# Performance work log

Measured on AMD Instinct MI355X. Metric: run time of the kernel, lower is better.

## Reference

```python
import jax, jax.numpy as jnp
import numpy as np

N_NODES = 100000
N_EDGES = 1600000
N_GRAPHS = 1000
H = 4

def _ln(x, g, b, eps=1e-5):
    m = x.mean(-1, keepdims=True)
    v = ((x - m) ** 2).mean(-1, keepdims=True)
    return (x - m) / jnp.sqrt(v + eps) * g + b

def _gat(x, src, dst, W, att_src, att_dst, bias, C):
    # PyG GATConv (self-loops already appended to src/dst): per-edge scores,
    # segment softmax over incoming edges of each dst node, scatter-add aggregation.
    N = x.shape[0]
    h = (x @ W.T).reshape(N, H, C)                      # [N,H,C]
    a_s = (h * att_src[None]).sum(-1)                   # [N,H]
    a_d = (h * att_dst[None]).sum(-1)                   # [N,H]
    e = jax.nn.leaky_relu(a_s[src] + a_d[dst], 0.2)     # [E,H]
    m = jax.ops.segment_max(e, dst, num_segments=N)
    w = jnp.exp(e - m[dst])
    denom = jax.ops.segment_sum(w, dst, num_segments=N)
    alpha = w / denom[dst]
    out = jax.ops.segment_sum(alpha[:, :, None] * h[src], dst, num_segments=N)
    return out.reshape(N, H * C) + bias

def _mha_len1(y, in_w, in_b, out_w, out_b, d):
    # seq_len==1 (x.unsqueeze(0)): softmax over a single key is identically 1,
    # so MHA(y,y,y) == out_proj(v_proj(y)). Exactly the original math.
    v = y @ in_w[2 * d:3 * d].T + in_b[2 * d:3 * d]
    return v @ out_w.T + out_b

def _forward(x, edge_index, batch, fc_feat_w, fc_feat_b,
             gat1_w, gat1_as, gat1_ad, gat1_b,
             gat2_w, gat2_as, gat2_ad, gat2_b,
             enc_in_w, enc_in_b, enc_out_w, enc_out_b,
             enc_f1_w, enc_f1_b, enc_f2_w, enc_f2_b,
             enc_ln1_g, enc_ln1_b, enc_ln2_g, enc_ln2_b,
             dec_sa_in_w, dec_sa_in_b, dec_sa_out_w, dec_sa_out_b,
             dec_ca_in_w, dec_ca_in_b, dec_ca_out_w, dec_ca_out_b,
             dec_f1_w, dec_f1_b, dec_f2_w, dec_f2_b,
             dec_ln1_g, dec_ln1_b, dec_ln2_g, dec_ln2_b, dec_ln3_g, dec_ln3_b,
             fc_w, fc_b):
    N = x.shape[0]
    d = 16 * H  # 64
    loop = jnp.arange(N, dtype=edge_index.dtype)
    src = jnp.concatenate([edge_index[0], loop])  # add_self_loops=True (PyG default)
    dst = jnp.concatenate([edge_index[1], loop])
    h = x @ fc_feat_w.T + fc_feat_b                     # feature_fc: [N,8]
    h = jax.nn.leaky_relu(_gat(h, src, dst, gat1_w, gat1_as, gat1_ad, gat1_b, 32), 0.01)
    h = jax.nn.leaky_relu(_gat(h, src, dst, gat2_w, gat2_as, gat2_ad, gat2_b, 16), 0.01)
    y = h  # [N,64]; transformer sees (L=1, B=N, E=64)
    for i in range(2):  # encoder layers
        a = _mha_len1(y, enc_in_w[i], enc_in_b[i], enc_out_w[i], enc_out_b[i], d)
        y = _ln(y + a, enc_ln1_g[i], enc_ln1_b[i])
        f = jax.nn.relu(y @ enc_f1_w[i].T + enc_f1_b[i]) @ enc_f2_w[i].T + enc_f2_b[i]
        y = _ln(y + f, enc_ln2_g[i], enc_ln2_b[i])
    for i in range(2):  # decoder layers (memory == tgt)
        a = _mha_len1(y, dec_sa_in_w[i], dec_sa_in_b[i], dec_sa_out_w[i], dec_sa_out_b[i], d)
        y = _ln(y + a, dec_ln1_g[i], dec_ln1_b[i])
        a = _mha_len1(y, dec_ca_in_w[i], dec_ca_in_b[i], dec_ca_out_w[i], dec_ca_out_b[i], d)
        y = _ln(y + a, dec_ln2_g[i], dec_ln2_b[i])
        f = jax.nn.relu(y @ dec_f1_w[i].T + dec_f1_b[i]) @ dec_f2_w[i].T + dec_f2_b[i]
        y = _ln(y + f, dec_ln3_g[i], dec_ln3_b[i])
    sums = jax.ops.segment_sum(y, batch, num_segments=N_GRAPHS)
    cnts = jax.ops.segment_sum(jnp.ones((N,), y.dtype), batch, num_segments=N_GRAPHS)
    pooled = sums / jnp.maximum(cnts, 1.0)[:, None]     # global_mean_pool
    return pooled @ fc_w.T + fc_b

def setup_inputs() -> dict:
    key = jax.random.key(0)
    ks = iter(jax.random.split(key, 64))
    p = lambda *s: jax.random.normal(next(ks), s, dtype=jnp.float32) * 0.1
    d = 64
    inp = {
        'x': jax.random.normal(next(ks), (N_NODES, 4), dtype=jnp.float32),
        'edge_index': jax.random.randint(next(ks), (2, N_EDGES), 0, N_NODES, dtype=jnp.int32),
        'batch': jnp.sort(jax.random.randint(next(ks), (N_NODES,), 0, N_GRAPHS, dtype=jnp.int32)),
        'fc_feat_w': p(8, 4), 'fc_feat_b': p(8),
        'gat1_w': p(128, 8), 'gat1_as': p(H, 32), 'gat1_ad': p(H, 32), 'gat1_b': p(128),
        'gat2_w': p(64, 128), 'gat2_as': p(H, 16), 'gat2_ad': p(H, 16), 'gat2_b': p(64),
        'enc_in_w': p(2, 3 * d, d), 'enc_in_b': p(2, 3 * d), 'enc_out_w': p(2, d, d), 'enc_out_b': p(2, d),
        'enc_f1_w': p(2, 256, d), 'enc_f1_b': p(2, 256), 'enc_f2_w': p(2, d, 256), 'enc_f2_b': p(2, d),
        'enc_ln1_g': jnp.ones((2, d)), 'enc_ln1_b': jnp.zeros((2, d)),
        'enc_ln2_g': jnp.ones((2, d)), 'enc_ln2_b': jnp.zeros((2, d)),
        'dec_sa_in_w': p(2, 3 * d, d), 'dec_sa_in_b': p(2, 3 * d), 'dec_sa_out_w': p(2, d, d), 'dec_sa_out_b': p(2, d),
        'dec_ca_in_w': p(2, 3 * d, d), 'dec_ca_in_b': p(2, 3 * d), 'dec_ca_out_w': p(2, d, d), 'dec_ca_out_b': p(2, d),
        'dec_f1_w': p(2, 256, d), 'dec_f1_b': p(2, 256), 'dec_f2_w': p(2, d, 256), 'dec_f2_b': p(2, d),
        'dec_ln1_g': jnp.ones((2, d)), 'dec_ln1_b': jnp.zeros((2, d)),
        'dec_ln2_g': jnp.ones((2, d)), 'dec_ln2_b': jnp.zeros((2, d)),
        'dec_ln3_g': jnp.ones((2, d)), 'dec_ln3_b': jnp.zeros((2, d)),
        'fc_w': p(33, d), 'fc_b': p(33),
    }
    return inp

def reference(x, edge_index, batch, fc_feat_w, fc_feat_b,
              gat1_w, gat1_as, gat1_ad, gat1_b,
              gat2_w, gat2_as, gat2_ad, gat2_b,
              enc_in_w, enc_in_b, enc_out_w, enc_out_b,
              enc_f1_w, enc_f1_b, enc_f2_w, enc_f2_b,
              enc_ln1_g, enc_ln1_b, enc_ln2_g, enc_ln2_b,
              dec_sa_in_w, dec_sa_in_b, dec_sa_out_w, dec_sa_out_b,
              dec_ca_in_w, dec_ca_in_b, dec_ca_out_w, dec_ca_out_b,
              dec_f1_w, dec_f1_b, dec_f2_w, dec_f2_b,
              dec_ln1_g, dec_ln1_b, dec_ln2_g, dec_ln2_b, dec_ln3_g, dec_ln3_b,
              fc_w, fc_b):
    return _forward(x, edge_index, batch, fc_feat_w, fc_feat_b,
                    gat1_w, gat1_as, gat1_ad, gat1_b,
                    gat2_w, gat2_as, gat2_ad, gat2_b,
                    enc_in_w, enc_in_b, enc_out_w, enc_out_b,
                    enc_f1_w, enc_f1_b, enc_f2_w, enc_f2_b,
                    enc_ln1_g, enc_ln1_b, enc_ln2_g, enc_ln2_b,
                    dec_sa_in_w, dec_sa_in_b, dec_sa_out_w, dec_sa_out_b,
                    dec_ca_in_w, dec_ca_in_b, dec_ca_out_w, dec_ca_out_b,
                    dec_f1_w, dec_f1_b, dec_f2_w, dec_f2_b,
                    dec_ln1_g, dec_ln1_b, dec_ln2_g, dec_ln2_b, dec_ln3_g, dec_ln3_b,
                    fc_w, fc_b)
```

## Files before the change

### kernel.cpp

```cpp
#include <hip/hip_runtime.h>

#define NN 100000
#define NE 1600000
#define NG 1000
#define ETOT (NE + NN)
#define NODES_PER_GRP 12500

typedef _Float16 f16x8 __attribute__((ext_vector_type(8)));
typedef _Float16 f16x4 __attribute__((ext_vector_type(4)));
typedef _Float16 f16x2 __attribute__((ext_vector_type(2)));
typedef float f32x16 __attribute__((ext_vector_type(16)));
#define XROW 72

__global__ void k_h1(const float* __restrict__ x, const float* __restrict__ ffw,
                     const float* __restrict__ ffb, const float* __restrict__ g1w,
                     const float* __restrict__ asw, const float* __restrict__ adw,
                     _Float16* __restrict__ h1p, float* __restrict__ asp,
                     float* __restrict__ ad_, int* __restrict__ deg) {
    int tid = blockIdx.x * 256 + threadIdx.x;
    if (tid < NN) deg[tid] = 0;
    int n = __builtin_amdgcn_readfirstlane(tid >> 6);
    int jp = threadIdx.x & 63;
    float xv[4];
#pragma unroll
    for (int k = 0; k < 4; k++) xv[k] = x[n * 4 + k];
    float h0[8];
#pragma unroll
    for (int o = 0; o < 8; o++) {
        float a = ffb[o];
#pragma unroll
        for (int k = 0; k < 4; k++) a = fmaf(xv[k], ffw[o * 4 + k], a);
        h0[o] = a;
    }
    const float* w0 = g1w + jp * 8;
    const float* w1 = g1w + (jp + 64) * 8;
    float a0 = 0.f, a1 = 0.f;
#pragma unroll
    for (int k = 0; k < 8; k++) { a0 = fmaf(h0[k], w0[k], a0); a1 = fmaf(h0[k], w1[k], a1); }
    f16x2 r; r[0] = (_Float16)a0; r[1] = (_Float16)a1;
    *(f16x2*)(h1p + ((size_t)n * 64 + jp) * 2) = r;
    float p0 = a0 * asw[jp], p1 = a1 * asw[jp + 64];
    float d0 = a0 * adw[jp], d1 = a1 * adw[jp + 64];
#pragma unroll
    for (int m = 1; m <= 16; m <<= 1) {
        p0 += __shfl_xor(p0, m, 64); p1 += __shfl_xor(p1, m, 64);
        d0 += __shfl_xor(d0, m, 64); d1 += __shfl_xor(d1, m, 64);
    }
    if ((jp & 31) == 0) {
        int half = jp >> 5;
        *(float2*)(asp + n * 4 + half * 2) = make_float2(p0, p1);
        ad_[n * 4 + half] = d0;
        ad_[n * 4 + 2 + half] = d1;
    }
}

#define CLD(q) int ee##q = e + q * stride; \
               int d##q = (ee##q < NE) ? __builtin_nontemporal_load(ei + NE + ee##q) : -1;
#define CAT(q) if (d##q >= lo && d##q < hi) atomicAdd(&deg[d##q], 1);
__global__ void k_count(const int* __restrict__ ei, int* __restrict__ deg) {
    int g = blockIdx.x & 7;
    int bi = blockIdx.x >> 3;
    int nb = gridDim.x >> 3;
    int lo = g * NODES_PER_GRP, hi = lo + NODES_PER_GRP;
    int stride = nb * 256;
    for (int e = bi * 256 + threadIdx.x; e < NE; e += 8 * stride) {
        CLD(0) CLD(1) CLD(2) CLD(3) CLD(4) CLD(5) CLD(6) CLD(7)
        CAT(0) CAT(1) CAT(2) CAT(3) CAT(4) CAT(5) CAT(6) CAT(7)
    }
}

__global__ void k_scan1(const int* __restrict__ deg, int* __restrict__ offs, int* __restrict__ bsum) {
    __shared__ int s[1024];
    int tid = threadIdx.x;
    int i = blockIdx.x * 1024 + tid;
    int v = (i < NN) ? deg[i] + 1 : 0;
    s[tid] = v;
    __syncthreads();
    for (int d = 1; d < 1024; d <<= 1) {
        int t = 0;
        if (tid >= d) t = s[tid - d];
        __syncthreads();
        if (tid >= d) s[tid] += t;
        __syncthreads();
    }
    if (i < NN) offs[i] = s[tid] - v;
    if (tid == 1023) bsum[blockIdx.x] = s[tid];
}

__global__ void k_scan2(int* __restrict__ bsum) {
    __shared__ int s[128];
    int tid = threadIdx.x;
    int v = (tid < 98) ? bsum[tid] : 0;
    s[tid] = v;
    __syncthreads();
    for (int d = 1; d < 128; d <<= 1) {
        int t = 0;
        if (tid >= d) t = s[tid - d];
        __syncthreads();
        if (tid >= d) s[tid] += t;
        __syncthreads();
    }
    bsum[tid] = s[tid] - v;
}

__global__ void k_scan3(int* __restrict__ offs, const int* __restrict__ bsum, int* __restrict__ cur,
                        int* __restrict__ srcs) {
    int i = blockIdx.x * 1024 + threadIdx.x;
    if (i < NN) {
        int v = offs[i] + bsum[blockIdx.x];
        offs[i] = v;
        cur[i] = v + 1;
        srcs[v] = i;
    }
    if (i == 0) offs[NN] = ETOT;
}

#define SLD(q) int ee##q = e + q * stride; int d##q = -1, s##q = 0; \
               if (ee##q < NE) { d##q = __builtin_nontemporal_load(ei + NE + ee##q); \
                                 s##q = __builtin_nontemporal_load(ei + ee##q); }
#define SAT(q) if (d##q >= lo && d##q < hi) { int p = atomicAdd(&cur[d##q], 1); srcs[p] = s##q; }
__global__ void k_scatter(const int* __restrict__ ei, int* __restrict__ cur,
                          int* __restrict__ srcs) {
    int g = blockIdx.x & 7;
    int bi = blockIdx.x >> 3;
    int nb = gridDim.x >> 3;
    int lo = g * NODES_PER_GRP, hi = lo + NODES_PER_GRP;
    int stride = nb * 256;
    for (int e = bi * 256 + threadIdx.x; e < NE; e += 8 * stride) {
        SLD(0) SLD(1) SLD(2) SLD(3) SLD(4) SLD(5) SLD(6) SLD(7)
        SAT(0) SAT(1) SAT(2) SAT(3) SAT(4) SAT(5) SAT(6) SAT(7)
    }
}

__global__ void k_ew1(const int* __restrict__ offs, const int* __restrict__ srcs,
                      const float* __restrict__ asp, const float* __restrict__ ad_,
                      uint2* __restrict__ ew) {
    int t = blockIdx.x * 256 + threadIdx.x;
    int d = t >> 4, li = t & 15;
    if (d >= NN) return;
    int off = offs[d], deg = offs[d + 1] - off;
    float4 b = *(const float4*)(ad_ + d * 4);
    for (int j = li; j < deg; j += 16) {
        int s = srcs[off + j];
        float4 a = *(const float4*)(asp + s * 4);
        float e0 = a.x + b.x; e0 = fmaxf(e0, 0.2f * e0);
        float e2 = a.y + b.z; e2 = fmaxf(e2, 0.2f * e2);
        float e1 = a.z + b.y; e1 = fmaxf(e1, 0.2f * e1);
        float e3 = a.w + b.w; e3 = fmaxf(e3, 0.2f * e3);
        union { unsigned u; _Float16 h[2]; } c0, c1;
        c0.h[0] = (_Float16)__expf(e0); c0.h[1] = (_Float16)__expf(e2);
        c1.h[0] = (_Float16)__expf(e1); c1.h[1] = (_Float16)__expf(e3);
        uint2 o; o.x = c0.u; o.y = c1.u;
        ew[off + j] = o;
    }
}

__global__ void k_ew2(const int* __restrict__ offs, const int* __restrict__ srcs,
                      const float* __restrict__ as_, const float* __restrict__ ad_,
                      uint2* __restrict__ ew) {
    int t = blockIdx.x * 256 + threadIdx.x;
    int d = t >> 4, li = t & 15;
    if (d >= NN) return;
    int off = offs[d], deg = offs[d + 1] - off;
    float4 b = *(const float4*)(ad_ + d * 4);
    for (int j = li; j < deg; j += 16) {
        int s = srcs[off + j];
        float4 a = *(const float4*)(as_ + s * 4);
        float e0 = a.x + b.x; e0 = fmaxf(e0, 0.2f * e0);
        float e1 = a.y + b.y; e1 = fmaxf(e1, 0.2f * e1);
        float e2 = a.z + b.z; e2 = fmaxf(e2, 0.2f * e2);
        float e3 = a.w + b.w; e3 = fmaxf(e3, 0.2f * e3);
        union { unsigned u; _Float16 h[2]; } c0, c1;
        c0.h[0] = (_Float16)__expf(e0); c0.h[1] = (_Float16)__expf(e1);
        c1.h[0] = (_Float16)__expf(e2); c1.h[1] = (_Float16)__expf(e3);
        uint2 o; o.x = c0.u; o.y = c1.u;
        ew[off + j] = o;
    }
}

#define G1LD(q)  int s##q = sp[j + q]; uint2 e##q = wp[j + q];
#define G1LDM(q) int jj##q = j + q; int jc##q = jj##q < deg ? jj##q : deg - 1; \
                 int s##q = sp[jc##q]; uint2 e##q = wp[jc##q]; \
                 if (jj##q >= deg) { e##q.x = 0u; e##q.y = 0u; }
#define G1GA(q)  f16x2 p##q = *(const f16x2*)(h1p + (size_t)s##q * 128 + lane * 2);
#define G1AC(q, W0, W1, A0, A1) { \
    union { unsigned u; _Float16 h[2]; } c; c.u = hA ? e##q.y : e##q.x; \
    float w0 = (float)c.h[0], w1 = (float)c.h[1]; \
    W0 += w0; W1 += w1; \
    A0 = fmaf(w0, (float)p##q[0], A0); A1 = fmaf(w1, (float)p##q[1], A1); }

__global__ void k_gat1(const int* __restrict__ offs, const int* __restrict__ srcs,
                       const uint2* __restrict__ ew, const _Float16* __restrict__ h1p,
                       const float* __restrict__ bias, _Float16* __restrict__ g1h) {
    int wid = __builtin_amdgcn_readfirstlane((blockIdx.x * 256 + threadIdx.x) >> 6);
    int lane = threadIdx.x & 63;
    if (wid >= NN) return;
    int off = offs[wid];
    int deg = offs[wid + 1] - off;
    int hA = lane >> 5;
    const int* sp = srcs + off;
    const uint2* wp = ew + off;
    float ws0 = 0.f, ws1 = 0.f, ac0 = 0.f, ac1 = 0.f;
    float ws0b = 0.f, ws1b = 0.f, ac0b = 0.f, ac1b = 0.f;
    int j = 0;
    for (; j + 8 <= deg; j += 8) {
        G1LD(0) G1LD(1) G1LD(2) G1LD(3) G1LD(4) G1LD(5) G1LD(6) G1LD(7)
        G1GA(0) G1GA(1) G1GA(2) G1GA(3) G1GA(4) G1GA(5) G1GA(6) G1GA(7)
        G1AC(0, ws0, ws1, ac0, ac1)     G1AC(1, ws0b, ws1b, ac0b, ac1b)
        G1AC(2, ws0, ws1, ac0, ac1)     G1AC(3, ws0b, ws1b, ac0b, ac1b)
        G1AC(4, ws0, ws1, ac0, ac1)     G1AC(5, ws0b, ws1b, ac0b, ac1b)
        G1AC(6, ws0, ws1, ac0, ac1)     G1AC(7, ws0b, ws1b, ac0b, ac1b)
    }
    if (j < deg) {
        G1LDM(0) G1LDM(1) G1LDM(2) G1LDM(3) G1LDM(4) G1LDM(5) G1LDM(6) G1LDM(7)
        G1GA(0) G1GA(1) G1GA(2) G1GA(3) G1GA(4) G1GA(5) G1GA(6) G1GA(7)
        G1AC(0, ws0, ws1, ac0, ac1)     G1AC(1, ws0b, ws1b, ac0b, ac1b)
        G1AC(2, ws0, ws1, ac0, ac1)     G1AC(3, ws0b, ws1b, ac0b, ac1b)
        G1AC(4, ws0, ws1, ac0, ac1)     G1AC(5, ws0b, ws1b, ac0b, ac1b)
        G1AC(6, ws0, ws1, ac0, ac1)     G1AC(7, ws0b, ws1b, ac0b, ac1b)
    }
    ws0 += ws0b; ws1 += ws1b; ac0 += ac0b; ac1 += ac1b;
    float v0 = ac0 / ws0 + bias[lane];      v0 = fmaxf(v0, 0.01f * v0);
    float v1 = ac1 / ws1 + bias[lane + 64]; v1 = fmaxf(v1, 0.01f * v1);
    g1h[(size_t)wid * 128 + lane] = (_Float16)v0;
    g1h[(size_t)wid * 128 + lane + 64] = (_Float16)v1;
}

#define G2LD(q)  int s##q = sp[j + q]; uint2 e##q = wp[j + q];
#define G2LDM(q) int jj##q = j + q; int jc##q = jj##q < deg ? jj##q : deg - 1; \
                 int s##q = sp[jc##q]; uint2 e##q = wp[jc##q]; \
                 if (jj##q >= deg) { e##q.x = 0u; e##q.y = 0u; }
#define G2GA(q)  float hv##q = (float)h2h[(size_t)s##q * 64 + lane];
#define G2AC(q, W, A) { \
    unsigned sel = (hd & 2) ? e##q.y : e##q.x; \
    union { unsigned u; _Float16 h[2]; } c; c.u = sel >> sh; \
    float w = (float)c.h[0]; W += w; A = fmaf(w, hv##q, A); }

__global__ void k_gat2(const int* __restrict__ offs, const int* __restrict__ srcs,
                       const uint2* __restrict__ ew, const _Float16* __restrict__ h2h,
                       const float* __restrict__ bias, _Float16* __restrict__ g2h) {
    int wid = __builtin_amdgcn_readfirstlane((blockIdx.x * 256 + threadIdx.x) >> 6);
    int lane = threadIdx.x & 63;
    if (wid >= NN) return;
    int off = offs[wid];
    int deg = offs[wid + 1] - off;
    int hd = lane >> 4;
    int sh = (hd & 1) * 16;
    const int* sp = srcs + off;
    const uint2* wp = ew + off;
    float ws = 0.f, ac = 0.f, wsb = 0.f, acb = 0.f;
    int j = 0;
    for (; j + 8 <= deg; j += 8) {
        G2LD(0) G2LD(1) G2LD(2) G2LD(3) G2LD(4) G2LD(5) G2LD(6) G2LD(7)
        G2GA(0) G2GA(1) G2GA(2) G2GA(3) G2GA(4) G2GA(5) G2GA(6) G2GA(7)
        G2AC(0, ws, ac)  G2AC(1, wsb, acb)
        G2AC(2, ws, ac)  G2AC(3, wsb, acb)
        G2AC(4, ws, ac)  G2AC(5, wsb, acb)
        G2AC(6, ws, ac)  G2AC(7, wsb, acb)
    }
    if (j < deg) {
        G2LDM(0) G2LDM(1) G2LDM(2) G2LDM(3) G2LDM(4) G2LDM(5) G2LDM(6) G2LDM(7)
        G2GA(0) G2GA(1) G2GA(2) G2GA(3) G2GA(4) G2GA(5) G2GA(6) G2GA(7)
        G2AC(0, ws, ac)  G2AC(1, wsb, acb)
        G2AC(2, ws, ac)  G2AC(3, wsb, acb)
        G2AC(4, ws, ac)  G2AC(5, wsb, acb)
        G2AC(6, ws, ac)  G2AC(7, wsb, acb)
    }
    ws += wsb; ac += acb;
    float v = ac / ws + bias[lane]; v = fmaxf(v, 0.01f * v);
    g2h[(size_t)wid * 64 + lane] = (_Float16)v;
}

#define GROW 136
#define CROW 72
__global__ __launch_bounds__(256, 2) void k_h2m(const _Float16* __restrict__ g1h,
                                                const _Float16* __restrict__ apw2,
                                                const float* __restrict__ asw,
                                                const float* __restrict__ adw,
                                                _Float16* __restrict__ h2h,
                                                float* __restrict__ as_,
                                                float* __restrict__ ad_) {
    __shared__ _Float16 ls[4 * 32 * GROW];
    const int t = threadIdx.x;
    const int w = t >> 6, l = t & 63;
    const int col = l & 31, hf = l >> 5;
    const int wv = blockIdx.x * 4 + w;
    const int nb = wv * 32;
    if (nb >= NN) return;
    _Float16* g16 = ls + w * (32 * GROW);
    const int r = l >> 1, hb = l & 1;
    {
        int nr = nb + r; if (nr >= NN) nr = NN - 1;
        const _Float16* src = g1h + (size_t)nr * 128 + hb * 64;
        _Float16* dst = g16 + r * GROW + hb * 64;
#pragma unroll
        for (int q = 0; q < 8; q++)
            *(f16x8*)(dst + q * 8) = *(const f16x8*)(src + q * 8);
    }
    f16x8 bf[8];
#pragma unroll
    for (int ks = 0; ks < 8; ks++)
        bf[ks] = *(const f16x8*)(g16 + col * GROW + ks * 16 + hf * 8);
    f32x16 acc0, acc1;
#pragma unroll
    for (int i = 0; i < 16; i++) { acc0[i] = 0.f; acc1[i] = 0.f; }
#pragma unroll
    for (int ks = 0; ks < 8; ks++) {
        f16x8 a0 = *(const f16x8*)(apw2 + ((0 * 8 + ks) * 64 + l) * 8);
        f16x8 a1 = *(const f16x8*)(apw2 + ((1 * 8 + ks) * 64 + l) * 8);
        acc0 = __builtin_amdgcn_mfma_f32_32x32x16_f16(a0, bf[ks], acc0, 0, 0, 0);
        acc1 = __builtin_amdgcn_mfma_f32_32x32x16_f16(a1, bf[ks], acc1, 0, 0, 0);
    }
    {
        float pa0 = 0.f, pa1 = 0.f, pa2 = 0.f, pa3 = 0.f;
        float pd0 = 0.f, pd1 = 0.f, pd2 = 0.f, pd3 = 0.f;
#pragma unroll
        for (int rg = 0; rg < 4; rg++)
#pragma unroll
            for (int i = 0; i < 4; i++) {
                int rr = rg * 4 + i;
                int f = i + rg * 8 + hf * 4;
                float h0v = (float)(_Float16)acc0[rr];
                float h1v = (float)(_Float16)acc1[rr];
                float s0 = asw[f], d0v = adw[f];
                float s1 = asw[32 + f], d1v = adw[32 + f];
                if (rg < 2) { pa0 = fmaf(h0v, s0, pa0); pd0 = fmaf(h0v, d0v, pd0);
                              pa2 = fmaf(h1v, s1, pa2); pd2 = fmaf(h1v, d1v, pd2); }
                else        { pa1 = fmaf(h0v, s0, pa1); pd1 = fmaf(h0v, d0v, pd1);
                              pa3 = fmaf(h1v, s1, pa3); pd3 = fmaf(h1v, d1v, pd3); }
            }
        pa0 += __shfl_xor(pa0, 32, 64); pa1 += __shfl_xor(pa1, 32, 64);
        pa2 += __shfl_xor(pa2, 32, 64); pa3 += __shfl_xor(pa3, 32, 64);
        pd0 += __shfl_xor(pd0, 32, 64); pd1 += __shfl_xor(pd1, 32, 64);
        pd2 += __shfl_xor(pd2, 32, 64); pd3 += __shfl_xor(pd3, 32, 64);
        if (hf == 0 && nb + col < NN) {
            *(float4*)(as_ + (size_t)(nb + col) * 4) = make_float4(pa0, pa1, pa2, pa3);
            *(float4*)(ad_ + (size_t)(nb + col) * 4) = make_float4(pd0, pd1, pd2, pd3);
        }
    }
    _Float16* c16 = g16;
#pragma unroll
    for (int rg = 0; rg < 4; rg++) {
        f16x4 h0, h1;
#pragma unroll
        for (int i = 0; i < 4; i++) { h0[i] = (_Float16)acc0[rg * 4 + i]; h1[i] = (_Float16)acc1[rg * 4 + i]; }
        *(f16x4*)(c16 + col * CROW + rg * 8 + hf * 4) = h0;
        *(f16x4*)(c16 + col * CROW + 32 + rg * 8 + hf * 4) = h1;
    }
    if (nb + r < NN) {
        _Float16* dst = h2h + (size_t)(nb + r) * 64 + hb * 32;
        const _Float16* srow = c16 + r * CROW + hb * 32;
#pragma unroll
        for (int q = 0; q < 4; q++)
            *(f16x8*)(dst + q * 8) = *(const f16x8*)(srow + q * 8);
    }
}

#define APK_F1 24576
#define APK_F2 90112
#define APK_TOT 155648
__global__ void k_prep(const float* __restrict__ enc_in_w, const float* __restrict__ enc_in_b,
                       const float* __restrict__ enc_out_w, const float* __restrict__ enc_out_b,
                       const float* __restrict__ sa_in_w, const float* __restrict__ sa_in_b,
                       const float* __restrict__ sa_out_w, const float* __restrict__ sa_out_b,
                       const float* __restrict__ ca_in_w, const float* __restrict__ ca_in_b,
                       const float* __restrict__ ca_out_w, const float* __restrict__ ca_out_b,
                       const float* __restrict__ ef1, const float* __restrict__ df1,
                       const float* __restrict__ ef2, const float* __restrict__ df2,
                       const float* __restrict__ g2w,
                       _Float16* __restrict__ apk, float* __restrict__ fb,
                       _Float16* __restrict__ apw2) {
    int gt = blockIdx.x * 256 + threadIdx.x;
    if (gt < 24576) {
        int tid = gt;
        int p = tid >> 12, rr = tid & 4095, j = rr >> 6, k = rr & 63;
        int li = p & 1;
        const float *iw, *ib, *ow, *ob;
        if (p < 2)      { iw = enc_in_w + li * 12288; ib = enc_in_b + li * 192; ow = enc_out_w + li * 4096; ob = enc_out_b + li * 64; }
        else if (p < 4) { iw = sa_in_w + li * 12288;  ib = sa_in_b + li * 192;  ow = sa_out_w + li * 4096;  ob = sa_out_b + li * 64; }
        else            { iw = ca_in_w + li * 12288;  ib = ca_in_b + li * 192;  ow = ca_out_w + li * 4096;  ob = ca_out_b + li * 64; }
        float a = 0.f;
        for (int m = 0; m < 64; m++) a = fmaf(ow[j * 64 + m], iw[(128 + m) * 64 + k], a);
        int l = ((k >> 3) & 1) * 32 + (j & 31);
        apk[p * 4096 + (((j >> 5) * 4 + (k >> 4)) * 64 + l) * 8 + (k & 7)] = (_Float16)a;
        if (k == 0) {
            float fa = ob[j];
            for (int m = 0; m < 64; m++) fa = fmaf(ow[j * 64 + m], ib[128 + m], fa);
            fb[p * 64 + j] = fa;
        }
    } else {
        int tid = gt - 24576;
        if (tid < 65536) {
            int pl = tid >> 14, idx = tid & 16383;
            int mt = idx >> 11, ks = (idx >> 9) & 3, l = (idx >> 3) & 63, d = idx & 7;
            int m = mt * 32 + (l & 31), k = ks * 16 + (l >> 5) * 8 + d;
            const float* f1 = (pl < 2) ? ef1 + pl * 16384 : df1 + (pl - 2) * 16384;
            apk[APK_F1 + pl * 16384 + idx] = (_Float16)f1[m * 64 + k];
        } else if (tid < 131072) {
            int rr = tid - 65536;
            int pl = rr >> 14, idx = rr & 16383;
            int mt = idx >> 13, ks = (idx >> 9) & 15, l = (idx >> 3) & 63, d = idx & 7;
            int m = mt * 32 + (l & 31), k = ks * 16 + (l >> 5) * 8 + d;
            const float* f2 = (pl < 2) ? ef2 + pl * 16384 : df2 + (pl - 2) * 16384;
            apk[APK_F2 + pl * 16384 + idx] = (_Float16)f2[m * 256 + k];
        } else {
            int rr = tid - 131072;
            int mtks = rr >> 9, l = (rr >> 3) & 63, d = rr & 7;
            int mt = mtks >> 3, ks = mtks & 7;
            int m = mt * 32 + (l & 31), k = ks * 16 + (l >> 5) * 8 + d;
            apw2[rr] = (_Float16)g2w[m * 128 + k];
        }
    }
}

struct XQ {
    const _Float16* apk; const float* fb;
    const float* ef1b; const float* ef2b; const float* df1b; const float* df2b;
    const float* el1g; const float* el1b; const float* el2g; const float* el2b;
    const float* dl1g; const float* dl1b; const float* dl2g; const float* dl2b;
    const float* dl3g; const float* dl3b;
};

__device__ __forceinline__ void xstore(_Float16* xw, const float y[4][16], int col, int hf) {
#pragma unroll
    for (int nt = 0; nt < 2; nt++)
#pragma unroll
        for (int mt = 0; mt < 2; mt++)
#pragma unroll
            for (int rg = 0; rg < 4; rg++) {
                f16x4 h4;
#pragma unroll
                for (int i = 0; i < 4; i++) h4[i] = (_Float16)y[mt * 2 + nt][rg * 4 + i];
                *(f16x4*)(xw + (nt * 32 + col) * XROW + mt * 32 + rg * 8 + hf * 4) = h4;
            }
}

__device__ __forceinline__ void loadbf(const _Float16* xw, f16x8 bf[2][4], int col, int hf) {
#pragma unroll
    for (int nt = 0; nt < 2; nt++)
#pragma unroll
        for (int ks = 0; ks < 4; ks++)
            bf[nt][ks] = *(const f16x8*)(xw + (nt * 32 + col) * XROW + ks * 16 + hf * 8);
}

__device__ __forceinline__ void lnw(float y[4][16], const float* g, const float* b, int hf) {
#pragma unroll
    for (int nt = 0; nt < 2; nt++) {
        float s = 0.f, q = 0.f;
#pragma unroll
        for (int mt = 0; mt < 2; mt++)
#pragma unroll
            for (int r = 0; r < 16; r++) { float v = y[mt * 2 + nt][r]; s += v; q = fmaf(v, v, q); }
        s += __shfl_xor(s, 32, 64);
        q += __shfl_xor(q, 32, 64);
        float m = s * 0.015625f;
        float var = fmaf(q, 0.015625f, -m * m);
        float rs = rsqrtf(var + 1e-5f);
#pragma unroll
        for (int mt = 0; mt < 2; mt++)
#pragma unroll
            for (int rg = 0; rg < 4; rg++) {
                float4 g4 = *(const float4*)(g + mt * 32 + rg * 8 + hf * 4);
                float4 b4 = *(const float4*)(b + mt * 32 + rg * 8 + hf * 4);
                float* yp = &y[mt * 2 + nt][rg * 4];
                yp[0] = fmaf((yp[0] - m) * rs, g4.x, b4.x);
                yp[1] = fmaf((yp[1] - m) * rs, g4.y, b4.y);
                yp[2] = fmaf((yp[2] - m) * rs, g4.z, b4.z);
                yp[3] = fmaf((yp[3] - m) * rs, g4.w, b4.w);
            }
    }
}

__global__ __launch_bounds__(64, 4) void k_xform(const _Float16* __restrict__ yin,
                                                 float* __restrict__ yout, XQ P) {
    __shared__ _Float16 xs[64 * XROW];
    __shared__ _Float16 wb[8192];
    const int t = threadIdx.x;
    const int l = t;
    const int col = l & 31, hf = l >> 5;
    _Float16* xw = xs;
    const int nb = blockIdx.x * 64;
    const int nn0 = nb + col, nn1 = nb + 32 + col;
    const int nc0 = nn0 < NN ? nn0 : NN - 1;
    const int nc1 = nn1 < NN ? nn1 : NN - 1;

    float y[4][16];
#pragma unroll
    for (int mt = 0; mt < 2; mt++)
#pragma unroll
        for (int nt = 0; nt < 2; nt++) {
            const _Float16* src = yin + (size_t)(nt ? nc1 : nc0) * 64 + mt * 32 + hf * 4;
#pragma unroll
            for (int rg = 0; rg < 4; rg++) {
                f16x4 v = *(const f16x4*)(src + rg * 8);
#pragma unroll
                for (int i = 0; i < 4; i++) y[mt * 2 + nt][rg * 4 + i] = (float)v[i];
            }
        }
    f16x8 bf[2][4];
    xstore(xw, y, col, hf);
    loadbf(xw, bf, col, hf);

#pragma unroll 1
    for (int layer = 0; layer < 4; layer++) {
        const bool enc = layer < 2;
        const int li = enc ? layer : layer - 2;
        const int nat = enc ? 1 : 2;
        const int pl = enc ? layer : 2 + li;
        const _Float16* apF1 = P.apk + APK_F1 + pl * 16384;
        const _Float16* apF2 = P.apk + APK_F2 + pl * 16384;
#pragma unroll 1
        for (int at = 0; at < nat; at++) {
            const int p = enc ? layer : (at == 0 ? 2 + li : 4 + li);
            const _Float16* apA = P.apk + p * 4096;
#pragma unroll
            for (int i = 0; i < 8; i++)
                *(f16x8*)(wb + (t + i * 64) * 8) = *(const f16x8*)(apA + (t + i * 64) * 8);
            const float* fbp = P.fb + p * 64;
            f32x16 acc[4];
#pragma unroll
            for (int mt = 0; mt < 2; mt++) {
                f32x16 a;
#pragma unroll
                for (int rg = 0; rg < 4; rg++) {
                    float4 b4 = *(const float4*)(fbp + mt * 32 + rg * 8 + hf * 4);
                    a[rg * 4 + 0] = b4.x; a[rg * 4 + 1] = b4.y; a[rg * 4 + 2] = b4.z; a[rg * 4 + 3] = b4.w;
                }
                acc[mt * 2 + 0] = a; acc[mt * 2 + 1] = a;
            }
#pragma unroll
            for (int mt = 0; mt < 2; mt++)
#pragma unroll
                for (int ks = 0; ks < 4; ks++) {
                    f16x8 af = *(const f16x8*)(wb + ((mt * 4 + ks) * 64 + l) * 8);
                    acc[mt * 2 + 0] = __builtin_amdgcn_mfma_f32_32x32x16_f16(af, bf[0][ks], acc[mt * 2 + 0], 0, 0, 0);
                    acc[mt * 2 + 1] = __builtin_amdgcn_mfma_f32_32x32x16_f16(af, bf[1][ks], acc[mt * 2 + 1], 0, 0, 0);
                }
#pragma unroll
            for (int ti = 0; ti < 4; ti++)
#pragma unroll
                for (int r = 0; r < 16; r++) y[ti][r] += acc[ti][r];
            const float *g, *b;
            if (enc)          { g = P.el1g + li * 64; b = P.el1b + li * 64; }
            else if (at == 0) { g = P.dl1g + li * 64; b = P.dl1b + li * 64; }
            else              { g = P.dl2g + li * 64; b = P.dl2b + li * 64; }
            lnw(y, g, b, hf);
            xstore(xw, y, col, hf);
            loadbf(xw, bf, col, hf);
        }
        const float* f1bp = (enc ? P.ef1b : P.df1b) + li * 256;
        const float* f2bp = (enc ? P.ef2b : P.df2b) + li * 64;
        f32x16 out[4];
#pragma unroll
        for (int mt = 0; mt < 2; mt++) {
            f32x16 a;
#pragma unroll
            for (int rg = 0; rg < 4; rg++) {
                float4 b4 = *(const float4*)(f2bp + mt * 32 + rg * 8 + hf * 4);
                a[rg * 4 + 0] = b4.x; a[rg * 4 + 1] = b4.y; a[rg * 4 + 2] = b4.z; a[rg * 4 + 3] = b4.w;
            }
            out[mt * 2 + 0] = a; out[mt * 2 + 1] = a;
        }
#pragma unroll 1
        for (int c = 0; c < 4; c++) {
#pragma unroll
            for (int i = 0; i < 8; i++)
                *(f16x8*)(wb + (t + i * 64) * 8) = *(const f16x8*)(apF1 + c * 4096 + (t + i * 64) * 8);
#pragma unroll
            for (int i = 0; i < 4; i++) {
                *(f16x8*)(wb + 4096 + (t + i * 64) * 8) = *(const f16x8*)(apF2 + c * 2048 + (t + i * 64) * 8);
                *(f16x8*)(wb + 6144 + (t + i * 64) * 8) = *(const f16x8*)(apF2 + 8192 + c * 2048 + (t + i * 64) * 8);
            }
            f32x16 ha[4];
#pragma unroll
            for (int hmt = 0; hmt < 2; hmt++) {
                f32x16 a;
#pragma unroll
                for (int rg = 0; rg < 4; rg++) {
                    float4 b4 = *(const float4*)(f1bp + c * 64 + hmt * 32 + rg * 8 + hf * 4);
                    a[rg * 4 + 0] = b4.x; a[rg * 4 + 1] = b4.y; a[rg * 4 + 2] = b4.z; a[rg * 4 + 3] = b4.w;
                }
                ha[hmt * 2 + 0] = a; ha[hmt * 2 + 1] = a;
            }
#pragma unroll
            for (int hmt = 0; hmt < 2; hmt++)
#pragma unroll
                for (int ks = 0; ks < 4; ks++) {
                    f16x8 af = *(const f16x8*)(wb + ((hmt * 4 + ks) * 64 + l) * 8);
                    ha[hmt * 2 + 0] = __builtin_amdgcn_mfma_f32_32x32x16_f16(af, bf[0][ks], ha[hmt * 2 + 0], 0, 0, 0);
                    ha[hmt * 2 + 1] = __builtin_amdgcn_mfma_f32_32x32x16_f16(af, bf[1][ks], ha[hmt * 2 + 1], 0, 0, 0);
                }
#pragma unroll
            for (int nt = 0; nt < 2; nt++)
#pragma unroll
                for (int hmt = 0; hmt < 2; hmt++)
#pragma unroll
                    for (int rg = 0; rg < 4; rg++) {
                        f16x4 h4;
#pragma unroll
                        for (int i = 0; i < 4; i++)
                            h4[i] = (_Float16)fmaxf(ha[hmt * 2 + nt][rg * 4 + i], 0.f);
                        *(f16x4*)(xw + (nt * 32 + col) * XROW + hmt * 32 + rg * 8 + hf * 4) = h4;
                    }
#pragma unroll
            for (int ksl = 0; ksl < 4; ksl++) {
                f16x8 hbf0 = *(const f16x8*)(xw + col * XROW + ksl * 16 + hf * 8);
                f16x8 hbf1 = *(const f16x8*)(xw + (32 + col) * XROW + ksl * 16 + hf * 8);
#pragma unroll
                for (int mt = 0; mt < 2; mt++) {
                    f16x8 af = *(const f16x8*)(wb + 4096 + mt * 2048 + (ksl * 64 + l) * 8);
                    out[mt * 2 + 0] = __builtin_amdgcn_mfma_f32_32x32x16_f16(af, hbf0, out[mt * 2 + 0], 0, 0, 0);
                    out[mt * 2 + 1] = __builtin_amdgcn_mfma_f32_32x32x16_f16(af, hbf1, out[mt * 2 + 1], 0, 0, 0);
                }
            }
        }
#pragma unroll
        for (int ti = 0; ti < 4; ti++)
#pragma unroll
            for (int r = 0; r < 16; r++) y[ti][r] += out[ti][r];
        const float* g2 = (enc ? P.el2g : P.dl3g) + li * 64;
        const float* b2 = (enc ? P.el2b : P.dl3b) + li * 64;
        lnw(y, g2, b2, hf);
        if (layer < 3) {
            xstore(xw, y, col, hf);
            loadbf(xw, bf, col, hf);
        }
    }
#pragma unroll
    for (int mt = 0; mt < 2; mt++)
#pragma unroll
        for (int nt = 0; nt < 2; nt++) {
            int n = nt ? nn1 : nn0;
            if (n < NN) {
                float* dst = yout + (size_t)n * 64 + mt * 32 + hf * 4;
#pragma unroll
                for (int rg = 0; rg < 4; rg++) {
                    const float* yp = &y[mt * 2 + nt][rg * 4];
                    *(float4*)(dst + rg * 8) = make_float4(yp[0], yp[1], yp[2], yp[3]);
                }
            }
        }
}

__global__ void k_pool(const float* __restrict__ y, const int* __restrict__ batch,
                       const float* __restrict__ fcw, const float* __restrict__ fcb,
                       float* __restrict__ out) {
    int b = blockIdx.x;
    int t = threadIdx.x;
    int ch = t & 63, r = t >> 6;
    int lo = 0, hi = NN;
    while (lo < hi) { int mid = (lo + hi) >> 1; if (batch[mid] < b) lo = mid + 1; else hi = mid; }
    int st = lo;
    hi = NN;
    while (lo < hi) { int mid = (lo + hi) >> 1; if (batch[mid] < b + 1) lo = mid + 1; else hi = mid; }
    int en = lo;
    float s = 0.f;
    for (int i = st + r; i < en; i += 4) s += y[(size_t)i * 64 + ch];
    __shared__ float red[256];
    __shared__ float pl[64];
    red[t] = s;
    __syncthreads();
    if (t < 64) {
        float tot = red[t] + red[t + 64] + red[t + 128] + red[t + 192];
        int cnt = en - st; if (cnt < 1) cnt = 1;
        pl[t] = tot / (float)cnt;
    }
    __syncthreads();
    if (t < 33) {
        const float* wv = fcw + t * 64;
        float a0 = 0.f, a1 = 0.f, a2 = 0.f, a3 = 0.f;
#pragma unroll
        for (int k = 0; k < 16; k++) {
            a0 = fmaf(pl[4 * k], wv[4 * k], a0);
            a1 = fmaf(pl[4 * k + 1], wv[4 * k + 1], a1);
            a2 = fmaf(pl[4 * k + 2], wv[4 * k + 2], a2);
            a3 = fmaf(pl[4 * k + 3], wv[4 * k + 3], a3);
        }
        out[b * 33 + t] = fcb[t] + (a0 + a1) + (a2 + a3);
    }
}

extern "C" void kernel_launch(void* const* d_in, const int* in_sizes, int n_in,
                              void* d_out, int out_size, void* d_ws, size_t ws_size,
                              hipStream_t stream) {
    (void)in_sizes; (void)n_in; (void)out_size; (void)ws_size;
    char* ws = (char*)d_ws;
    size_t o = 0;
    auto A = [&](size_t b) { size_t r = o; o += (b + 255) & ~(size_t)255; return r; };
    _Float16* h1p = (_Float16*)(ws + A((size_t)NN * 128 * 2));
    _Float16* h2h = (_Float16*)(ws + A((size_t)NN * 64 * 2));
    _Float16* g1h = (_Float16*)(ws + A((size_t)NN * 128 * 2));
    _Float16* g2h = (_Float16*)(ws + A((size_t)NN * 64 * 2));
    float* f_y   = (float*)(ws + A((size_t)NN * 64 * 4));
    float* f_asp = (float*)(ws + A((size_t)NN * 4 * 4));
    float* f_ad1 = (float*)(ws + A((size_t)NN * 4 * 4));
    float* f_as2 = (float*)(ws + A((size_t)NN * 4 * 4));
    float* f_ad2 = (float*)(ws + A((size_t)NN * 4 * 4));
    int* i_off   = (int*)(ws + A((size_t)(NN + 1) * 4));
    int* i_cur   = (int*)(ws + A((size_t)NN * 4));
    int* i_deg   = (int*)(ws + A((size_t)NN * 4));
    int* i_bsum  = (int*)(ws + A((size_t)1024 * 4));
    int* i_srcs  = (int*)(ws + A((size_t)ETOT * 4));
    uint2* e_w   = (uint2*)(ws + A((size_t)ETOT * 8));
    float* f_fb  = (float*)(ws + A((size_t)6 * 64 * 4));
    _Float16* f_apk = (_Float16*)(ws + A((size_t)APK_TOT * 2));
    _Float16* apw2  = (_Float16*)(ws + A((size_t)8192 * 2));

    const float* x   = (const float*)d_in[0];
    const int* ei    = (const int*)d_in[1];
    const int* batch = (const int*)d_in[2];
    #define F32(i) ((const float*)d_in[i])

    k_h1<<<NN * 64 / 256, 256, 0, stream>>>(x, F32(3), F32(4), F32(5), F32(6), F32(7),
                                            h1p, f_asp, f_ad1, i_deg);
    k_count<<<8 * 256, 256, 0, stream>>>(ei, i_deg);
    k_scan1<<<98, 1024, 0, stream>>>(i_deg, i_off, i_bsum);
    k_scan2<<<1, 128, 0, stream>>>(i_bsum);
    k_scan3<<<98, 1024, 0, stream>>>(i_off, i_bsum, i_cur, i_srcs);
    k_scatter<<<8 * 256, 256, 0, stream>>>(ei, i_cur, i_srcs);
    k_ew1<<<NN * 16 / 256, 256, 0, stream>>>(i_off, i_srcs, f_asp, f_ad1, e_w);
    k_gat1<<<NN * 64 / 256, 256, 0, stream>>>(i_off, i_srcs, e_w, h1p, F32(8), g1h);
    k_prep<<<640, 256, 0, stream>>>(F32(13), F32(14), F32(15), F32(16),
                                    F32(25), F32(26), F32(27), F32(28),
                                    F32(29), F32(30), F32(31), F32(32),
                                    F32(17), F32(33), F32(19), F32(35), F32(9),
                                    f_apk, f_fb, apw2);
    k_h2m<<<(NN / 32 + 3) / 4, 256, 0, stream>>>(g1h, apw2, F32(10), F32(11), h2h, f_as2, f_ad2);
    k_ew2<<<NN * 16 / 256, 256, 0, stream>>>(i_off, i_srcs, f_as2, f_ad2, e_w);
    k_gat2<<<NN * 64 / 256, 256, 0, stream>>>(i_off, i_srcs, e_w, h2h, F32(12), g2h);
    XQ Q;
    Q.apk = f_apk; Q.fb = f_fb;
    Q.ef1b = F32(18); Q.ef2b = F32(20);
    Q.df1b = F32(34); Q.df2b = F32(36);
    Q.el1g = F32(21); Q.el1b = F32(22); Q.el2g = F32(23); Q.el2b = F32(24);
    Q.dl1g = F32(37); Q.dl1b = F32(38); Q.dl2g = F32(39); Q.dl2b = F32(40);
    Q.dl3g = F32(41); Q.dl3b = F32(42);
    k_xform<<<(NN + 63) / 64, 64, 0, stream>>>(g2h, f_y, Q);
    k_pool<<<NG, 256, 0, stream>>>(f_y, batch, F32(43), F32(44), (float*)d_out);
    #undef F32
}
```

Before: 579.8 us.

## Merge CSR count/scatter with independent kernels and widen xform blocks

The edge-degree count is folded into the node feature projection kernel as extra blocks, and the CSR scatter is merged with the weight-packing prep kernel, so fewer launches run back to back and independent work shares one grid. Degree zeroing moves to a hipMemsetAsync. k_xform now uses 256-thread blocks of four waves that share the staged weight tiles in LDS, cutting redundant global-to-LDS weight copies per node tile, but it adds __syncthreads barriers and more shared memory per block, which may lower occupancy.

```diff
diff --git a/kernel.cpp b/kernel.cpp
--- a/kernel.cpp
+++ b/kernel.cpp
@@ -5,6 +5,7 @@
 #define NG 1000
 #define ETOT (NE + NN)
 #define NODES_PER_GRP 12500
+#define CSR_NB 256
 
 typedef _Float16 f16x8 __attribute__((ext_vector_type(8)));
 typedef _Float16 f16x4 __attribute__((ext_vector_type(4)));
@@ -12,13 +13,27 @@
 typedef float f32x16 __attribute__((ext_vector_type(16)));
 #define XROW 72
 
-__global__ void k_h1(const float* __restrict__ x, const float* __restrict__ ffw,
-                     const float* __restrict__ ffb, const float* __restrict__ g1w,
-                     const float* __restrict__ asw, const float* __restrict__ adw,
-                     _Float16* __restrict__ h1p, float* __restrict__ asp,
-                     float* __restrict__ ad_, int* __restrict__ deg) {
-    int tid = blockIdx.x * 256 + threadIdx.x;
-    if (tid < NN) deg[tid] = 0;
+__global__ void k_cnth1(const int* __restrict__ ei, int* __restrict__ deg,
+                        const float* __restrict__ x, const float* __restrict__ ffw,
+                        const float* __restrict__ ffb, const float* __restrict__ g1w,
+                        const float* __restrict__ asw, const float* __restrict__ adw,
+                        _Float16* __restrict__ h1p, float* __restrict__ asp,
+                        float* __restrict__ ad_) {
+    if (blockIdx.x < 8 * CSR_NB) {
+        int g = blockIdx.x & 7;
+        int bi = blockIdx.x >> 3;
+        int lo = g * NODES_PER_GRP, hi = lo + NODES_PER_GRP;
+        const int stride = CSR_NB * 256;
+#define CLD(q) int ee##q = e + q * stride; \
+               int d##q = (ee##q < NE) ? __builtin_nontemporal_load(ei + NE + ee##q) : -1;
+#define CAT(q) if (d##q >= lo && d##q < hi) atomicAdd(&deg[d##q], 1);
+        for (int e = bi * 256 + threadIdx.x; e < NE; e += 8 * stride) {
+            CLD(0) CLD(1) CLD(2) CLD(3) CLD(4) CLD(5) CLD(6) CLD(7)
+            CAT(0) CAT(1) CAT(2) CAT(3) CAT(4) CAT(5) CAT(6) CAT(7)
+        }
+        return;
+    }
+    int tid = (blockIdx.x - 8 * CSR_NB) * 256 + threadIdx.x;
     int n = __builtin_amdgcn_readfirstlane(tid >> 6);
     int jp = threadIdx.x & 63;
     float xv[4];
@@ -51,21 +66,6 @@
         *(float2*)(asp + n * 4 + half * 2) = make_float2(p0, p1);
         ad_[n * 4 + half] = d0;
         ad_[n * 4 + 2 + half] = d1;
-    }
-}
-
-#define CLD(q) int ee##q = e + q * stride; \
-               int d##q = (ee##q < NE) ? __builtin_nontemporal_load(ei + NE + ee##q) : -1;
-#define CAT(q) if (d##q >= lo && d##q < hi) atomicAdd(&deg[d##q], 1);
-__global__ void k_count(const int* __restrict__ ei, int* __restrict__ deg) {
-    int g = blockIdx.x & 7;
-    int bi = blockIdx.x >> 3;
-    int nb = gridDim.x >> 3;
-    int lo = g * NODES_PER_GRP, hi = lo + NODES_PER_GRP;
-    int stride = nb * 256;
-    for (int e = bi * 256 + threadIdx.x; e < NE; e += 8 * stride) {
-        CLD(0) CLD(1) CLD(2) CLD(3) CLD(4) CLD(5) CLD(6) CLD(7)
-        CAT(0) CAT(1) CAT(2) CAT(3) CAT(4) CAT(5) CAT(6) CAT(7)
     }
 }
 
@@ -115,20 +115,77 @@
     if (i == 0) offs[NN] = ETOT;
 }
 
+#define APK_F1 24576
+#define APK_F2 90112
+#define APK_TOT 155648
+__global__ void k_scatprep(const int* __restrict__ ei, int* __restrict__ cur,
+                           int* __restrict__ srcs,
+                           const float* __restrict__ enc_in_w, const float* __restrict__ enc_in_b,
+                           const float* __restrict__ enc_out_w, const float* __restrict__ enc_out_b,
+                           const float* __restrict__ sa_in_w, const float* __restrict__ sa_in_b,
+                           const float* __restrict__ sa_out_w, const float* __restrict__ sa_out_b,
+                           const float* __restrict__ ca_in_w, const float* __restrict__ ca_in_b,
+                           const float* __restrict__ ca_out_w, const float* __restrict__ ca_out_b,
+                           const float* __restrict__ ef1, const float* __restrict__ df1,
+                           const float* __restrict__ ef2, const float* __restrict__ df2,
+                           const float* __restrict__ g2w,
+                           _Float16* __restrict__ apk, float* __restrict__ fb,
+                           _Float16* __restrict__ apw2) {
+    if (blockIdx.x < 8 * CSR_NB) {
+        int g = blockIdx.x & 7;
+        int bi = blockIdx.x >> 3;
+        int lo = g * NODES_PER_GRP, hi = lo + NODES_PER_GRP;
+        const int stride = CSR_NB * 256;
 #define SLD(q) int ee##q = e + q * stride; int d##q = -1, s##q = 0; \
                if (ee##q < NE) { d##q = __builtin_nontemporal_load(ei + NE + ee##q); \
                                  s##q = __builtin_nontemporal_load(ei + ee##q); }
 #define SAT(q) if (d##q >= lo && d##q < hi) { int p = atomicAdd(&cur[d##q], 1); srcs[p] = s##q; }
-__global__ void k_scatter(const int* __restrict__ ei, int* __restrict__ cur,
-                          int* __restrict__ srcs) {
-    int g = blockIdx.x & 7;
-    int bi = blockIdx.x >> 3;
-    int nb = gridDim.x >> 3;
-    int lo = g * NODES_PER_GRP, hi = lo + NODES_PER_GRP;
-    int stride = nb * 256;
-    for (int e = bi * 256 + threadIdx.x; e < NE; e += 8 * stride) {
-        SLD(0) SLD(1) SLD(2) SLD(3) SLD(4) SLD(5) SLD(6) SLD(7)
-        SAT(0) SAT(1) SAT(2) SAT(3) SAT(4) SAT(5) SAT(6) SAT(7)
+        for (int e = bi * 256 + threadIdx.x; e < NE; e += 8 * stride) {
+            SLD(0) SLD(1) SLD(2) SLD(3) SLD(4) SLD(5) SLD(6) SLD(7)
+            SAT(0) SAT(1) SAT(2) SAT(3) SAT(4) SAT(5) SAT(6) SAT(7)
+        }
+        return;
+    }
+    int gt = (blockIdx.x - 8 * CSR_NB) * 256 + threadIdx.x;
+    if (gt < 24576) {
+        int tid = gt;
+        int p = tid >> 12, rr = tid & 4095, j = rr >> 6, k = rr & 63;
+        int li = p & 1;
+        const float *iw, *ib, *ow, *ob;
+        if (p < 2)      { iw = enc_in_w + li * 12288; ib = enc_in_b + li * 192; ow = enc_out_w + li * 4096; ob = enc_out_b + li * 64; }
+        else if (p < 4) { iw = sa_in_w + li * 12288;  ib = sa_in_b + li * 192;  ow = sa_out_w + li * 4096;  ob = sa_out_b + li * 64; }
+        else            { iw = ca_in_w + li * 12288;  ib = ca_in_b + li * 192;  ow = ca_out_w + li * 4096;  ob = ca_out_b + li * 64; }
+        float a = 0.f;
+        for (int m = 0; m < 64; m++) a = fmaf(ow[j * 64 + m], iw[(128 + m) * 64 + k], a);
+        int l = ((k >> 3) & 1) * 32 + (j & 31);
+        apk[p * 4096 + (((j >> 5) * 4 + (k >> 4)) * 64 + l) * 8 + (k & 7)] = (_Float16)a;
+        if (k == 0) {
+            float fa = ob[j];
+            for (int m = 0; m < 64; m++) fa = fmaf(ow[j * 64 + m], ib[128 + m], fa);
+            fb[p * 64 + j] = fa;
+        }
+    } else {
+        int tid = gt - 24576;
+        if (tid < 65536) {
+            int pl = tid >> 14, idx = tid & 16383;
+            int mt = idx >> 11, ks = (idx >> 9) & 3, l = (idx >> 3) & 63, d = idx & 7;
+            int m = mt * 32 + (l & 31), k = ks * 16 + (l >> 5) * 8 + d;
+            const float* f1 = (pl < 2) ? ef1 + pl * 16384 : df1 + (pl - 2) * 16384;
+            apk[APK_F1 + pl * 16384 + idx] = (_Float16)f1[m * 64 + k];
+        } else if (tid < 131072) {
+            int rr = tid - 65536;
+            int pl = rr >> 14, idx = rr & 16383;
+            int mt = idx >> 13, ks = (idx >> 9) & 15, l = (idx >> 3) & 63, d = idx & 7;
+            int m = mt * 32 + (l & 31), k = ks * 16 + (l >> 5) * 8 + d;
+            const float* f2 = (pl < 2) ? ef2 + pl * 16384 : df2 + (pl - 2) * 16384;
+            apk[APK_F2 + pl * 16384 + idx] = (_Float16)f2[m * 256 + k];
+        } else {
+            int rr = tid - 131072;
+            int mtks = rr >> 9, l = (rr >> 3) & 63, d = rr & 7;
+            int mt = mtks >> 3, ks = mtks & 7;
+            int m = mt * 32 + (l & 31), k = ks * 16 + (l >> 5) * 8 + d;
+            apw2[rr] = (_Float16)g2w[m * 128 + k];
+        }
     }
 }
 
@@ -356,63 +413,6 @@
     }
 }
 
-#define APK_F1 24576
-#define APK_F2 90112
-#define APK_TOT 155648
-__global__ void k_prep(const float* __restrict__ enc_in_w, const float* __restrict__ enc_in_b,
-                       const float* __restrict__ enc_out_w, const float* __restrict__ enc_out_b,
-                       const float* __restrict__ sa_in_w, const float* __restrict__ sa_in_b,
-                       const float* __restrict__ sa_out_w, const float* __restrict__ sa_out_b,
-                       const float* __restrict__ ca_in_w, const float* __restrict__ ca_in_b,
-                       const float* __restrict__ ca_out_w, const float* __restrict__ ca_out_b,
-                       const float* __restrict__ ef1, const float* __restrict__ df1,
-                       const float* __restrict__ ef2, const float* __restrict__ df2,
-                       const float* __restrict__ g2w,
-                       _Float16* __restrict__ apk, float* __restrict__ fb,
-                       _Float16* __restrict__ apw2) {
-    int gt = blockIdx.x * 256 + threadIdx.x;
-    if (gt < 24576) {
-        int tid = gt;
-        int p = tid >> 12, rr = tid & 4095, j = rr >> 6, k = rr & 63;
-        int li = p & 1;
-        const float *iw, *ib, *ow, *ob;
-        if (p < 2)      { iw = enc_in_w + li * 12288; ib = enc_in_b + li * 192; ow = enc_out_w + li * 4096; ob = enc_out_b + li * 64; }
-        else if (p < 4) { iw = sa_in_w + li * 12288;  ib = sa_in_b + li * 192;  ow = sa_out_w + li * 4096;  ob = sa_out_b + li * 64; }
-        else            { iw = ca_in_w + li * 12288;  ib = ca_in_b + li * 192;  ow = ca_out_w + li * 4096;  ob = ca_out_b + li * 64; }
-        float a = 0.f;
-        for (int m = 0; m < 64; m++) a = fmaf(ow[j * 64 + m], iw[(128 + m) * 64 + k], a);
-        int l = ((k >> 3) & 1) * 32 + (j & 31);
-        apk[p * 4096 + (((j >> 5) * 4 + (k >> 4)) * 64 + l) * 8 + (k & 7)] = (_Float16)a;
-        if (k == 0) {
-            float fa = ob[j];
-            for (int m = 0; m < 64; m++) fa = fmaf(ow[j * 64 + m], ib[128 + m], fa);
-            fb[p * 64 + j] = fa;
-        }
-    } else {
-        int tid = gt - 24576;
-        if (tid < 65536) {
-            int pl = tid >> 14, idx = tid & 16383;
-            int mt = idx >> 11, ks = (idx >> 9) & 3, l = (idx >> 3) & 63, d = idx & 7;
-            int m = mt * 32 + (l & 31), k = ks * 16 + (l >> 5) * 8 + d;
-            const float* f1 = (pl < 2) ? ef1 + pl * 16384 : df1 + (pl - 2) * 16384;
-            apk[APK_F1 + pl * 16384 + idx] = (_Float16)f1[m * 64 + k];
-        } else if (tid < 131072) {
-            int rr = tid - 65536;
-            int pl = rr >> 14, idx = rr & 16383;
-            int mt = idx >> 13, ks = (idx >> 9) & 15, l = (idx >> 3) & 63, d = idx & 7;
-            int m = mt * 32 + (l & 31), k = ks * 16 + (l >> 5) * 8 + d;
-            const float* f2 = (pl < 2) ? ef2 + pl * 16384 : df2 + (pl - 2) * 16384;
-            apk[APK_F2 + pl * 16384 + idx] = (_Float16)f2[m * 256 + k];
-        } else {
-            int rr = tid - 131072;
-            int mtks = rr >> 9, l = (rr >> 3) & 63, d = rr & 7;
-            int mt = mtks >> 3, ks = mtks & 7;
-            int m = mt * 32 + (l & 31), k = ks * 16 + (l >> 5) * 8 + d;
-            apw2[rr] = (_Float16)g2w[m * 128 + k];
-        }
-    }
-}
-
 struct XQ {
     const _Float16* apk; const float* fb;
     const float* ef1b; const float* ef2b; const float* df1b; const float* df2b;
@@ -471,15 +471,15 @@
     }
 }
 
-__global__ __launch_bounds__(64, 4) void k_xform(const _Float16* __restrict__ yin,
-                                                 float* __restrict__ yout, XQ P) {
-    __shared__ _Float16 xs[64 * XROW];
+__global__ __launch_bounds__(256, 2) void k_xform(const _Float16* __restrict__ yin,
+                                                  float* __restrict__ yout, XQ P) {
+    __shared__ _Float16 xs[4 * 64 * XROW];
     __shared__ _Float16 wb[8192];
     const int t = threadIdx.x;
-    const int l = t;
+    const int w = t >> 6, l = t & 63;
     const int col = l & 31, hf = l >> 5;
-    _Float16* xw = xs;
-    const int nb = blockIdx.x * 64;
+    _Float16* xw = xs + w * (64 * XROW);
+    const int nb = blockIdx.x * 256 + w * 64;
     const int nn0 = nb + col, nn1 = nb + 32 + col;
     const int nc0 = nn0 < NN ? nn0 : NN - 1;
     const int nc1 = nn1 < NN ? nn1 : NN - 1;
@@ -506,16 +506,15 @@
         const bool enc = layer < 2;
         const int li = enc ? layer : layer - 2;
         const int nat = enc ? 1 : 2;
-        const int pl = enc ? layer : 2 + li;
-        const _Float16* apF1 = P.apk + APK_F1 + pl * 16384;
-        const _Float16* apF2 = P.apk + APK_F2 + pl * 16384;
 #pragma unroll 1
         for (int at = 0; at < nat; at++) {
             const int p = enc ? layer : (at == 0 ? 2 + li : 4 + li);
             const _Float16* apA = P.apk + p * 4096;
-#pragma unroll
-            for (int i = 0; i < 8; i++)
-                *(f16x8*)(wb + (t + i * 64) * 8) = *(const f16x8*)(apA + (t + i * 64) * 8);
+            __syncthreads();
+#pragma unroll
+            for (int i = 0; i < 2; i++)
+                *(f16x8*)(wb + (t + i * 256) * 8) = *(const f16x8*)(apA + (t + i * 256) * 8);
+            __syncthreads();
             const float* fbp = P.fb + p * 64;
             f32x16 acc[4];
 #pragma unroll
@@ -548,6 +547,9 @@
             xstore(xw, y, col, hf);
             loadbf(xw, bf, col, hf);
         }
+        const int pl = enc ? layer : 2 + li;
+        const _Float16* apF1 = P.apk + APK_F1 + pl * 16384;
+        const _Float16* apF2 = P.apk + APK_F2 + pl * 16384;
         const float* f1bp = (enc ? P.ef1b : P.df1b) + li * 256;
         const float* f2bp = (enc ? P.ef2b : P.df2b) + li * 64;
         f32x16 out[4];
@@ -563,14 +565,13 @@
         }
 #pragma unroll 1
         for (int c = 0; c < 4; c++) {
-#pragma unroll
-            for (int i = 0; i < 8; i++)
-                *(f16x8*)(wb + (t + i * 64) * 8) = *(const f16x8*)(apF1 + c * 4096 + (t + i * 64) * 8);
-#pragma unroll
-            for (int i = 0; i < 4; i++) {
-                *(f16x8*)(wb + 4096 + (t + i * 64) * 8) = *(const f16x8*)(apF2 + c * 2048 + (t + i * 64) * 8);
-                *(f16x8*)(wb + 6144 + (t + i * 64) * 8) = *(const f16x8*)(apF2 + 8192 + c * 2048 + (t + i * 64) * 8);
-            }
+            __syncthreads();
+#pragma unroll
+            for (int i = 0; i < 2; i++)
+                *(f16x8*)(wb + (t + i * 256) * 8) = *(const f16x8*)(apF1 + c * 4096 + (t + i * 256) * 8);
+            *(f16x8*)(wb + 4096 + t * 8) = *(const f16x8*)(apF2 + c * 2048 + t * 8);
+            *(f16x8*)(wb + 6144 + t * 8) = *(const f16x8*)(apF2 + 8192 + c * 2048 + t * 8);
+            __syncthreads();
             f32x16 ha[4];
 #pragma unroll
             for (int hmt = 0; hmt < 2; hmt++) {
@@ -711,20 +712,21 @@
     const int* batch = (const int*)d_in[2];
     #define F32(i) ((const float*)d_in[i])
 
-    k_h1<<<NN * 64 / 256, 256, 0, stream>>>(x, F32(3), F32(4), F32(5), F32(6), F32(7),
-                                            h1p, f_asp, f_ad1, i_deg);
-    k_count<<<8 * 256, 256, 0, stream>>>(ei, i_deg);
+    hipMemsetAsync(i_deg, 0, (size_t)NN * 4, stream);
+    k_cnth1<<<8 * CSR_NB + NN * 64 / 256, 256, 0, stream>>>(
+        ei, i_deg, x, F32(3), F32(4), F32(5), F32(6), F32(7), h1p, f_asp, f_ad1);
     k_scan1<<<98, 1024, 0, stream>>>(i_deg, i_off, i_bsum);
     k_scan2<<<1, 128, 0, stream>>>(i_bsum);
     k_scan3<<<98, 1024, 0, stream>>>(i_off, i_bsum, i_cur, i_srcs);
-    k_scatter<<<8 * 256, 256, 0, stream>>>(ei, i_cur, i_srcs);
+    k_scatprep<<<8 * CSR_NB + 640, 256, 0, stream>>>(
+        ei, i_cur, i_srcs,
+        F32(13), F32(14), F32(15), F32(16),
+        F32(25), F32(26), F32(27), F32(28),
+        F32(29), F32(30), F32(31), F32(32),
+        F32(17), F32(33), F32(19), F32(35), F32(9),
+        f_apk, f_fb, apw2);
     k_ew1<<<NN * 16 / 256, 256, 0, stream>>>(i_off, i_srcs, f_asp, f_ad1, e_w);
     k_gat1<<<NN * 64 / 256, 256, 0, stream>>>(i_off, i_srcs, e_w, h1p, F32(8), g1h);
-    k_prep<<<640, 256, 0, stream>>>(F32(13), F32(14), F32(15), F32(16),
-                                    F32(25), F32(26), F32(27), F32(28),
-                                    F32(29), F32(30), F32(31), F32(32),
-                                    F32(17), F32(33), F32(19), F32(35), F32(9),
-                                    f_apk, f_fb, apw2);
     k_h2m<<<(NN / 32 + 3) / 4, 256, 0, stream>>>(g1h, apw2, F32(10), F32(11), h2h, f_as2, f_ad2);
     k_ew2<<<NN * 16 / 256, 256, 0, stream>>>(i_off, i_srcs, f_as2, f_ad2, e_w);
     k_gat2<<<NN * 64 / 256, 256, 0, stream>>>(i_off, i_srcs, e_w, h2h, F32(12), g2h);
@@ -735,7 +737,7 @@
     Q.el1g = F32(21); Q.el1b = F32(22); Q.el2g = F32(23); Q.el2b = F32(24);
     Q.dl1g = F32(37); Q.dl1b = F32(38); Q.dl2g = F32(39); Q.dl2b = F32(40);
     Q.dl3g = F32(41); Q.dl3b = F32(42);
-    k_xform<<<(NN + 63) / 64, 64, 0, stream>>>(g2h, f_y, Q);
+    k_xform<<<(NN + 255) / 256, 256, 0, stream>>>(g2h, f_y, Q);
     k_pool<<<NG, 256, 0, stream>>>(f_y, batch, F32(43), F32(44), (float*)d_out);
     #undef F32
 }
```

Result: faster. 562.4 us (-3.0%).
